# Kernel tuning notes

Hardware: AMD Instinct MI355X
Metric: run time of the kernel (lower is better)

## Reference

```python
import jax, jax.numpy as jnp
import numpy as np

D_MODEL = 1024
D_INNER = 2048  # expand * d_model
D_STATE = 16
D_CONV = 4
DT_RANK = 64    # ceil(d_model / 16)
B_SZ, L_SEQ = 2, 1024


def setup_inputs() -> dict:
    key = jax.random.key(0)
    ks = jax.random.split(key, 8)
    s = lambda fan_in: 1.0 / np.sqrt(fan_in)
    x = jax.random.normal(ks[0], (B_SZ, L_SEQ, D_MODEL), dtype=jnp.float32)
    in_proj_w = jax.random.normal(ks[1], (2 * D_INNER, D_MODEL), jnp.float32) * s(D_MODEL)
    conv_w = jax.random.normal(ks[2], (D_INNER, 1, D_CONV), jnp.float32) * s(D_CONV)
    conv_b = jax.random.normal(ks[3], (D_INNER,), jnp.float32) * 0.02
    x_proj_w = jax.random.normal(ks[4], (DT_RANK + 2 * D_STATE, D_INNER), jnp.float32) * s(D_INNER)
    dt_proj_w = jax.random.normal(ks[5], (D_INNER, DT_RANK), jnp.float32) * s(DT_RANK)
    dt_proj_b = jax.random.normal(ks[6], (D_INNER,), jnp.float32) * 0.02
    A_log = jnp.broadcast_to(jnp.log(jnp.arange(1, D_STATE + 1, dtype=jnp.float32)), (D_INNER, D_STATE))
    D_param = jnp.ones((D_INNER,), jnp.float32)
    out_proj_w = jax.random.normal(ks[7], (D_MODEL, D_INNER), jnp.float32) * s(D_INNER)
    return dict(x=x, in_proj_w=in_proj_w, conv_w=conv_w, conv_b=conv_b,
                x_proj_w=x_proj_w, dt_proj_w=dt_proj_w, dt_proj_b=dt_proj_b,
                A_log=A_log, D_param=D_param, out_proj_w=out_proj_w)


def _mamba_forward(x, in_proj_w, conv_w, conv_b, x_proj_w, dt_proj_w, dt_proj_b, A_log, D_param, out_proj_w):
    B, L, _ = x.shape
    # in_proj: (B,L,2*d_inner) -> split into conv branch and gate
    xz = jnp.einsum('bld,ed->ble', x, in_proj_w)
    x_br, z = jnp.split(xz, 2, axis=-1)
    # depthwise causal conv1d (left pad d_conv-1, truncate to L == torch pad+slice)
    xc = jnp.transpose(x_br, (0, 2, 1))  # (B, d_inner, L)
    xc = jax.lax.conv_general_dilated(
        xc, conv_w, window_strides=(1,), padding=[(D_CONV - 1, 0)],
        dimension_numbers=('NCH', 'OIH', 'NCH'), feature_group_count=D_INNER)
    xc = xc + conv_b[None, :, None]
    u = jax.nn.silu(jnp.transpose(xc, (0, 2, 1)))  # (B, L, d_inner) = SSM input
    # input-dependent params
    proj = jnp.einsum('bld,ed->ble', u, x_proj_w)
    delta_raw, B_in, C_in = jnp.split(proj, [DT_RANK, DT_RANK + D_STATE], axis=-1)
    delta = jax.nn.softplus(jnp.einsum('blr,dr->bld', delta_raw, dt_proj_w) + dt_proj_b)
    A = -jnp.exp(A_log)  # (d_inner, d_state)

    def step(h, inp):
        d_t, b_t, c_t, u_t = inp  # (B,d_inner),(B,d_state),(B,d_state),(B,d_inner)
        dA = jnp.exp(d_t[:, :, None] * A)                       # (B,d_inner,d_state)
        h = dA * h + (d_t * u_t)[:, :, None] * b_t[:, None, :]  # ZOH-ish update
        y_t = jnp.einsum('bds,bs->bd', h, c_t) + D_param * u_t
        return h, y_t

    h0 = jnp.zeros((B, D_INNER, D_STATE), dtype=x.dtype)
    inputs = (jnp.swapaxes(delta, 0, 1), jnp.swapaxes(B_in, 0, 1),
              jnp.swapaxes(C_in, 0, 1), jnp.swapaxes(u, 0, 1))
    _, ys = jax.lax.scan(step, h0, inputs)  # (L, B, d_inner)
    y = jnp.swapaxes(ys, 0, 1) * jax.nn.silu(z)
    return jnp.einsum('ble,de->bld', y, out_proj_w)


def reference(x, in_proj_w, conv_w, conv_b, x_proj_w, dt_proj_w, dt_proj_b, A_log, D_param, out_proj_w):
    return _mamba_forward(x, in_proj_w, conv_w, conv_b, x_proj_w, dt_proj_w, dt_proj_b, A_log, D_param, out_proj_w)
```

## Files before the change

kernel.cpp:

```cpp
#include <hip/hip_runtime.h>
#include <hip/hip_bf16.h>

#define D_MODEL 1024
#define D_INNER 2048
#define D_STATE 16
#define D_CONV  4
#define DT_RANK 64
#define B_SZ    2
#define L_SEQ   1024
#define BL      (B_SZ * L_SEQ)
#define NPROJ   (DT_RANK + 2 * D_STATE)
#define CS      32
#define NC      (L_SEQ / CS)

typedef __attribute__((ext_vector_type(8))) short bf16x8;
typedef __attribute__((ext_vector_type(4))) float floatx4;
typedef unsigned short ushort_t;

__device__ __forceinline__ void mfma_bf16(floatx4& acc, bf16x8 a, bf16x8 b) {
    asm volatile("v_mfma_f32_16x16x32_bf16 %0, %1, %2, %0"
                 : "+v"(acc) : "v"(a), "v"(b));
}

__device__ __forceinline__ void cvt_hilo(float f, ushort_t& hi, ushort_t& lo) {
    __hip_bfloat16 h = __float2bfloat16(f);
    hi = *(ushort_t*)&h;
    __hip_bfloat16 l = __float2bfloat16(f - __bfloat162float(h));
    lo = *(ushort_t*)&l;
}

__device__ __forceinline__ void cvt_store4(float4 v, ushort_t* hi, ushort_t* lo) {
    ushort4 h, l;
    cvt_hilo(v.x, h.x, l.x);
    cvt_hilo(v.y, h.y, l.y);
    cvt_hilo(v.z, h.z, l.z);
    cvt_hilo(v.w, h.w, l.w);
    *(ushort4*)hi = h;
    *(ushort4*)lo = l;
}

#define N4_WI 1048576
#define N4_WO 524288
#define N4_WD 32768
#define N4_X  524288

__global__ __launch_bounds__(256) void cvt_static(
    const float* __restrict__ wi, ushort_t* wihi, ushort_t* wilo,
    const float* __restrict__ wo, ushort_t* wohi, ushort_t* wolo,
    const float* __restrict__ wd, ushort_t* wdhi, ushort_t* wdlo,
    const float* __restrict__ x,  ushort_t* xhi,  ushort_t* xlo)
{
    int i = blockIdx.x * 256 + threadIdx.x;
    const float* src; ushort_t *dh, *dl;
    if (i < N4_WI)                         { src = wi; dh = wihi; dl = wilo; }
    else if ((i -= N4_WI) < N4_WO)         { src = wo; dh = wohi; dl = wolo; }
    else if ((i -= N4_WO) < N4_WD)         { src = wd; dh = wdhi; dl = wdlo; }
    else { i -= N4_WD;                       src = x;  dh = xhi;  dl = xlo;  }
    float4 v = ((const float4*)src)[i];
    cvt_store4(v, dh + i * 4, dl + i * 4);
}

template <int TM, int TN, int EPI, int CVTA, int KSPLIT>
__global__ __launch_bounds__(256, 2) void gemm_pre(
    const ushort_t* __restrict__ Ahi, const ushort_t* __restrict__ Alo, int lda,
    const float* __restrict__ Af, int ldaf,
    const ushort_t* __restrict__ Bhi, const ushort_t* __restrict__ Blo, int ldb,
    float* __restrict__ C, int ldc, int K,
    const float* __restrict__ bias)
{
    constexpr int LDT = 32;
    constexpr int IT = TM / 32, JT = TN / 32;
    __shared__ __align__(16) ushort_t As[2][TM * LDT];
    __shared__ __align__(16) ushort_t Bs[2][TN * LDT];

    const int tid = threadIdx.x;
    const int bm = blockIdx.y * TM;
    const int bn = blockIdx.x * TN;
    const int kstart = (KSPLIT > 1) ? blockIdx.z * (K / KSPLIT) : 0;
    const int kend   = (KSPLIT > 1) ? kstart + K / KSPLIT : K;

    const int wave = tid >> 6;
    const int lane = tid & 63;
    const int wm = (wave >> 1) * (TM / 2);
    const int wn = (wave & 1) * (TN / 2);
    const int ml = lane & 15;
    const int q  = lane >> 4;

    floatx4 acc[IT][JT];
#pragma unroll
    for (int i = 0; i < IT; ++i)
#pragma unroll
        for (int j = 0; j < JT; ++j) acc[i][j] = (floatx4)0.f;

    for (int k0 = kstart; k0 < kend; k0 += 32) {
        __syncthreads();
        if (CVTA) {
            const int r  = tid >> 1;
            const int kh = (tid & 1) * 16;
            const int sw = (r >> 1) & 3;
            const int c0 = (tid & 1) * 2;
            ushort_t hi[16], lo[16];
#pragma unroll
            for (int c = 0; c < 4; ++c) {
                float4 v = *(const float4*)(Af + (size_t)(bm + r) * ldaf + k0 + kh + c * 4);
                cvt_store4(v, hi + c * 4, lo + c * 4);
            }
            const int p0 = (c0 ^ sw) * 8;
            const int p1 = ((c0 + 1) ^ sw) * 8;
            *(uint4*)&As[0][r * LDT + p0] = *(uint4*)(hi + 0);
            *(uint4*)&As[0][r * LDT + p1] = *(uint4*)(hi + 8);
            *(uint4*)&As[1][r * LDT + p0] = *(uint4*)(lo + 0);
            *(uint4*)&As[1][r * LDT + p1] = *(uint4*)(lo + 8);
        } else {
#pragma unroll
            for (int ci = 0; ci < TM / 64; ++ci) {
                const int flat = tid + 256 * ci;
                const int r = flat >> 2, c = flat & 3;
                const int p = (c ^ ((r >> 1) & 3)) * 8;
                *(uint4*)&As[0][r * LDT + p] =
                    *(const uint4*)(Ahi + (size_t)(bm + r) * lda + k0 + c * 8);
                *(uint4*)&As[1][r * LDT + p] =
                    *(const uint4*)(Alo + (size_t)(bm + r) * lda + k0 + c * 8);
            }
        }
#pragma unroll
        for (int ci = 0; ci < TN / 64; ++ci) {
            const int flat = tid + 256 * ci;
            const int r = flat >> 2, c = flat & 3;
            const int p = (c ^ ((r >> 1) & 3)) * 8;
            *(uint4*)&Bs[0][r * LDT + p] =
                *(const uint4*)(Bhi + (size_t)(bn + r) * ldb + k0 + c * 8);
            *(uint4*)&Bs[1][r * LDT + p] =
                *(const uint4*)(Blo + (size_t)(bn + r) * ldb + k0 + c * 8);
        }
        __syncthreads();

        bf16x8 ah[IT], al[IT], bh[JT], bl[JT];
#pragma unroll
        for (int i = 0; i < IT; ++i) {
            const int r = wm + i * 16 + ml;
            const int p = (q ^ ((r >> 1) & 3)) * 8;
            ah[i] = *(const bf16x8*)&As[0][r * LDT + p];
            al[i] = *(const bf16x8*)&As[1][r * LDT + p];
        }
#pragma unroll
        for (int j = 0; j < JT; ++j) {
            const int r = wn + j * 16 + ml;
            const int p = (q ^ ((r >> 1) & 3)) * 8;
            bh[j] = *(const bf16x8*)&Bs[0][r * LDT + p];
            bl[j] = *(const bf16x8*)&Bs[1][r * LDT + p];
        }
#pragma unroll
        for (int i = 0; i < IT; ++i)
#pragma unroll
            for (int j = 0; j < JT; ++j) {
                mfma_bf16(acc[i][j], ah[i], bh[j]);
                mfma_bf16(acc[i][j], ah[i], bl[j]);
                mfma_bf16(acc[i][j], al[i], bh[j]);
            }
    }

    asm volatile("s_nop 7\n\ts_nop 7\n\ts_nop 7" ::: "memory");

#pragma unroll
    for (int i = 0; i < IT; ++i)
#pragma unroll
        for (int j = 0; j < JT; ++j)
#pragma unroll
            for (int r = 0; r < 4; ++r) {
                const int row = bm + wm + i * 16 + q * 4 + r;
                const int col = bn + wn + j * 16 + ml;
                float v = acc[i][j][r];
                if (KSPLIT > 1) {
                    atomicAdd(C + (size_t)row * ldc + col, v);
                } else {
                    if (EPI == 1) {
                        v += bias[col];
                        v = (v > 20.f) ? v : log1pf(__expf(v));
                    }
                    C[(size_t)row * ldc + col] = v;
                }
            }
}

#define PKC 128
#define PSC 64

__global__ __launch_bounds__(256) void gemm_proj_conv(
    const float* __restrict__ xz,
    const float* __restrict__ conv_w,
    const float* __restrict__ conv_b,
    const float* __restrict__ Wp,
    float* __restrict__ proj,
    float* __restrict__ u_out)
{
    __shared__ float us[PSC][65];
    __shared__ float wsh[PSC][100];

    const int tid = threadIdx.x;
    const int bm = blockIdx.y * 64;
    const int kbase0 = blockIdx.x * PKC;

    const int tx = tid & 15;
    const int ty = tid >> 4;

    float acc[4][6];
#pragma unroll
    for (int i = 0; i < 4; ++i)
#pragma unroll
        for (int j = 0; j < 6; ++j) acc[i][j] = 0.f;

    for (int sc = 0; sc < PKC / PSC; ++sc) {
        const int kb = kbase0 + sc * PSC;
        __syncthreads();
#pragma unroll
        for (int i = 0; i < 4; ++i) {
            const int flat = tid + 256 * i;
            const int r  = flat >> 4;
            const int kk = (flat & 15) * 4;
            const int k  = kb + kk;
            const int rr = bm + r;
            const int t  = rr & (L_SEQ - 1);
            const float* base = xz + (size_t)rr * 4096 + k;
            float4 x0 = *(const float4*)(base);
            float4 x1 = (t >= 1) ? *(const float4*)(base - 4096)  : make_float4(0,0,0,0);
            float4 x2 = (t >= 2) ? *(const float4*)(base - 8192)  : make_float4(0,0,0,0);
            float4 x3 = (t >= 3) ? *(const float4*)(base - 12288) : make_float4(0,0,0,0);
            float4 cb = *(const float4*)(conv_b + k);
            float4 w0 = ((const float4*)conv_w)[k + 0];
            float4 w1 = ((const float4*)conv_w)[k + 1];
            float4 w2 = ((const float4*)conv_w)[k + 2];
            float4 w3 = ((const float4*)conv_w)[k + 3];
            float4 uo;
            { float a = cb.x + w0.x*x3.x + w0.y*x2.x + w0.z*x1.x + w0.w*x0.x;
              uo.x = a / (1.f + __expf(-a)); }
            { float a = cb.y + w1.x*x3.y + w1.y*x2.y + w1.z*x1.y + w1.w*x0.y;
              uo.y = a / (1.f + __expf(-a)); }
            { float a = cb.z + w2.x*x3.z + w2.y*x2.z + w2.z*x1.z + w2.w*x0.z;
              uo.z = a / (1.f + __expf(-a)); }
            { float a = cb.w + w3.x*x3.w + w3.y*x2.w + w3.z*x1.w + w3.w*x0.w;
              uo.w = a / (1.f + __expf(-a)); }
            us[kk + 0][r] = uo.x;
            us[kk + 1][r] = uo.y;
            us[kk + 2][r] = uo.z;
            us[kk + 3][r] = uo.w;
            *(float4*)(u_out + (size_t)rr * D_INNER + k) = uo;
        }
#pragma unroll
        for (int i = 0; i < 6; ++i) {
            const int flat = tid + 256 * i;
            const int r = flat >> 4;
            const int k4 = flat & 15;
            float4 v = *(const float4*)(Wp + (size_t)r * D_INNER + kb + k4 * 4);
            wsh[k4*4+0][r] = v.x; wsh[k4*4+1][r] = v.y;
            wsh[k4*4+2][r] = v.z; wsh[k4*4+3][r] = v.w;
        }
        __syncthreads();

#pragma unroll 8
        for (int kk = 0; kk < PSC; ++kk) {
            float a[4], b[6];
#pragma unroll
            for (int i = 0; i < 4; ++i) a[i] = us[kk][ty * 4 + i];
#pragma unroll
            for (int j = 0; j < 6; ++j) b[j] = wsh[kk][tx + 16 * j];
#pragma unroll
            for (int i = 0; i < 4; ++i)
#pragma unroll
                for (int j = 0; j < 6; ++j) acc[i][j] += a[i] * b[j];
        }
    }

#pragma unroll
    for (int i = 0; i < 4; ++i)
#pragma unroll
        for (int j = 0; j < 6; ++j)
            atomicAdd(proj + (size_t)(bm + ty * 4 + i) * NPROJ + tx + 16 * j,
                      acc[i][j]);
}

__global__ __launch_bounds__(256) void scan_phase_a(
    const float* __restrict__ xz,
    const float* __restrict__ u,
    const float* __restrict__ proj,
    const float* __restrict__ A_log,
    float* __restrict__ hloc,
    float* __restrict__ sumd)
{
    const int d = blockIdx.x * 256 + threadIdx.x;
    const int c = blockIdx.y;
    const int b = blockIdx.z;

    float a[D_STATE];
#pragma unroll
    for (int s = 0; s < D_STATE; ++s) a[s] = -__expf(A_log[d * D_STATE + s]);

    float h[D_STATE];
#pragma unroll
    for (int s = 0; s < D_STATE; ++s) h[s] = 0.f;
    float sd = 0.f;

    for (int t = c * CS; t < (c + 1) * CS; ++t) {
        const size_t bt = (size_t)b * L_SEQ + t;
        const float dv = xz[bt * (2 * D_INNER) + d];
        const float uv = u[bt * D_INNER + d];
        const float du = dv * uv;
        sd += dv;
        const float* pr = proj + bt * NPROJ;
#pragma unroll
        for (int s = 0; s < D_STATE; ++s)
            h[s] = __expf(dv * a[s]) * h[s] + du * pr[DT_RANK + s];
    }

    const size_t base = ((size_t)(b * NC + c) * D_STATE) * D_INNER + d;
#pragma unroll
    for (int s = 0; s < D_STATE; ++s) hloc[base + (size_t)s * D_INNER] = h[s];
    sumd[(size_t)(b * NC + c) * D_INNER + d] = sd;
}

__global__ __launch_bounds__(256) void scan_phase_b(
    const float* __restrict__ hloc,
    const float* __restrict__ sumd,
    const float* __restrict__ A_log,
    float* __restrict__ carry)
{
    const int d = blockIdx.x * 256 + threadIdx.x;
    const int b = blockIdx.y;

    float a[D_STATE];
#pragma unroll
    for (int s = 0; s < D_STATE; ++s) a[s] = -__expf(A_log[d * D_STATE + s]);

    float hc[D_STATE];
#pragma unroll
    for (int s = 0; s < D_STATE; ++s) {
        hc[s] = 0.f;
        carry[((size_t)(b * NC + 0) * D_STATE + s) * D_INNER + d] = 0.f;
    }

    for (int c = 1; c < NC; ++c) {
        const float sd = sumd[(size_t)(b * NC + c - 1) * D_INNER + d];
        const size_t pbase = ((size_t)(b * NC + c - 1) * D_STATE) * D_INNER + d;
        const size_t cbase = ((size_t)(b * NC + c) * D_STATE) * D_INNER + d;
#pragma unroll
        for (int s = 0; s < D_STATE; ++s) {
            const float P = __expf(a[s] * sd);
            hc[s] = P * hc[s] + hloc[pbase + (size_t)s * D_INNER];
            carry[cbase + (size_t)s * D_INNER] = hc[s];
        }
    }
}

__global__ __launch_bounds__(256) void scan_phase_c(
    const float* __restrict__ xz,
    const float* __restrict__ u,
    const float* __restrict__ proj,
    const float* __restrict__ A_log,
    const float* __restrict__ D_param,
    const float* __restrict__ carry,
    ushort_t* __restrict__ Yhi,
    ushort_t* __restrict__ Ylo)
{
    const int d = blockIdx.x * 256 + threadIdx.x;
    const int c = blockIdx.y;
    const int b = blockIdx.z;

    float a[D_STATE];
#pragma unroll
    for (int s = 0; s < D_STATE; ++s) a[s] = -__expf(A_log[d * D_STATE + s]);
    const float Dp = D_param[d];

    float h[D_STATE];
    const size_t cbase = ((size_t)(b * NC + c) * D_STATE) * D_INNER + d;
#pragma unroll
    for (int s = 0; s < D_STATE; ++s) h[s] = carry[cbase + (size_t)s * D_INNER];

    for (int t = c * CS; t < (c + 1) * CS; ++t) {
        const size_t bt = (size_t)b * L_SEQ + t;
        const float dv = xz[bt * (2 * D_INNER) + d];
        const float uv = u[bt * D_INNER + d];
        const float du = dv * uv;
        const float* pr = proj + bt * NPROJ;

        float acc = 0.f;
#pragma unroll
        for (int s = 0; s < D_STATE; ++s) {
            h[s] = __expf(dv * a[s]) * h[s] + du * pr[DT_RANK + s];
            acc += h[s] * pr[DT_RANK + D_STATE + s];
        }
        const float yv = acc + Dp * uv;

        const float zv = xz[bt * (2 * D_INNER) + D_INNER + d];
        const float gate = zv / (1.f + __expf(-zv));
        ushort_t hh, ll;
        cvt_hilo(yv * gate, hh, ll);
        Yhi[bt * D_INNER + d] = hh;
        Ylo[bt * D_INNER + d] = ll;
    }
}

extern "C" void kernel_launch(void* const* d_in, const int* in_sizes, int n_in,
                              void* d_out, int out_size, void* d_ws, size_t ws_size,
                              hipStream_t stream)
{
    const float* x         = (const float*)d_in[0];
    const float* in_proj_w = (const float*)d_in[1];
    const float* conv_w    = (const float*)d_in[2];
    const float* conv_b    = (const float*)d_in[3];
    const float* x_proj_w  = (const float*)d_in[4];
    const float* dt_proj_w = (const float*)d_in[5];
    const float* dt_proj_b = (const float*)d_in[6];
    const float* A_log     = (const float*)d_in[7];
    const float* D_param   = (const float*)d_in[8];
    const float* out_proj_w= (const float*)d_in[9];
    float* out = (float*)d_out;

    float* xz    = (float*)d_ws;
    float* u     = xz    + (size_t)BL * 4096;
    float* proj  = u     + (size_t)BL * 2048;
    float* sumd  = proj  + (size_t)BL * NPROJ;
    float* carry = sumd  + (size_t)B_SZ * NC * D_INNER;
    ushort_t* Wihi = (ushort_t*)(carry + (size_t)B_SZ * NC * D_STATE * D_INNER);
    ushort_t* Wilo = Wihi + (size_t)4096 * 1024;
    ushort_t* Wohi = Wilo + (size_t)4096 * 1024;
    ushort_t* Wolo = Wohi + (size_t)1024 * 2048;
    ushort_t* Wdhi = Wolo + (size_t)1024 * 2048;
    ushort_t* Wdlo = Wdhi + (size_t)2048 * 64;
    ushort_t* Xhi  = (ushort_t*)carry;
    ushort_t* Xlo  = Xhi + (size_t)BL * D_MODEL;
    float*    hloc = (float*)Wihi;
    ushort_t* Yhi  = Wihi;
    ushort_t* Ylo  = Wilo;

    dim3 blk(256);

    cvt_static<<<(N4_WI + N4_WO + N4_WD + N4_X) / 256, blk, 0, stream>>>(
        in_proj_w, Wihi, Wilo, out_proj_w, Wohi, Wolo,
        dt_proj_w, Wdhi, Wdlo, x, Xhi, Xlo);

    gemm_pre<128, 128, 0, 0, 1><<<dim3(4096 / 128, BL / 128), blk, 0, stream>>>(
        Xhi, Xlo, D_MODEL, nullptr, 0, Wihi, Wilo, D_MODEL,
        xz, 2 * D_INNER, D_MODEL, nullptr);

    hipMemsetAsync(proj, 0, (size_t)BL * NPROJ * sizeof(float), stream);
    gemm_proj_conv<<<dim3(D_INNER / PKC, BL / 64), blk, 0, stream>>>(
        xz, conv_w, conv_b, x_proj_w, proj, u);

    gemm_pre<128, 128, 1, 1, 1><<<dim3(D_INNER / 128, BL / 128), blk, 0, stream>>>(
        nullptr, nullptr, 0, proj, NPROJ, Wdhi, Wdlo, DT_RANK,
        xz, 2 * D_INNER, DT_RANK, dt_proj_b);

    scan_phase_a<<<dim3(D_INNER / 256, NC, B_SZ), blk, 0, stream>>>(
        xz, u, proj, A_log, hloc, sumd);
    scan_phase_b<<<dim3(D_INNER / 256, B_SZ), blk, 0, stream>>>(
        hloc, sumd, A_log, carry);
    scan_phase_c<<<dim3(D_INNER / 256, NC, B_SZ), blk, 0, stream>>>(
        xz, u, proj, A_log, D_param, carry, Yhi, Ylo);

    hipMemsetAsync(out, 0, (size_t)BL * D_MODEL * sizeof(float), stream);
    gemm_pre<128, 64, 0, 0, 2><<<dim3(D_MODEL / 64, BL / 128, 2), blk, 0, stream>>>(
        Yhi, Ylo, D_INNER, nullptr, 0, Wohi, Wolo, D_INNER,
        out, D_MODEL, D_INNER, nullptr);
}
```

Baseline: 337.4 us.

## Replace dt_proj MFMA GEMM with FP32 delta kernel and fuse zero fills

Swaps the split-bf16 MFMA GEMM for dt_proj (K=64), which converted proj to hi/lo inside the tile loader, for a plain FP32 kernel. Each thread keeps one dt_proj_w row in registers, loops over 16 staged proj rows, and applies bias and softplus. It also drops the dt_proj_w conversion from cvt_static and merges the two memset calls into one zero-fill kernel at the start. The goal is to cut launch and conversion overhead on a small-K GEMM. The cost is the 64-float register array per thread, and the FP32 FMAs run on vector ALUs instead of MFMA.

```diff
diff --git a/kernel.cpp b/kernel.cpp
--- a/kernel.cpp
+++ b/kernel.cpp
@@ -39,34 +39,41 @@
     *(ushort4*)lo = l;
 }
 
+#define Z4_PROJ (BL * NPROJ / 4)
+#define Z4_OUT  (BL * D_MODEL / 4)
+
+__global__ __launch_bounds__(256) void zero_buf(float* __restrict__ proj,
+                                                float* __restrict__ out)
+{
+    int i = blockIdx.x * 256 + threadIdx.x;
+    float4 z = make_float4(0.f, 0.f, 0.f, 0.f);
+    if (i < Z4_PROJ) ((float4*)proj)[i] = z;
+    else             ((float4*)out)[i - Z4_PROJ] = z;
+}
+
 #define N4_WI 1048576
 #define N4_WO 524288
-#define N4_WD 32768
 #define N4_X  524288
 
 __global__ __launch_bounds__(256) void cvt_static(
     const float* __restrict__ wi, ushort_t* wihi, ushort_t* wilo,
     const float* __restrict__ wo, ushort_t* wohi, ushort_t* wolo,
-    const float* __restrict__ wd, ushort_t* wdhi, ushort_t* wdlo,
     const float* __restrict__ x,  ushort_t* xhi,  ushort_t* xlo)
 {
     int i = blockIdx.x * 256 + threadIdx.x;
     const float* src; ushort_t *dh, *dl;
-    if (i < N4_WI)                         { src = wi; dh = wihi; dl = wilo; }
-    else if ((i -= N4_WI) < N4_WO)         { src = wo; dh = wohi; dl = wolo; }
-    else if ((i -= N4_WO) < N4_WD)         { src = wd; dh = wdhi; dl = wdlo; }
-    else { i -= N4_WD;                       src = x;  dh = xhi;  dl = xlo;  }
+    if (i < N4_WI)                 { src = wi; dh = wihi; dl = wilo; }
+    else if ((i -= N4_WI) < N4_WO) { src = wo; dh = wohi; dl = wolo; }
+    else { i -= N4_WO;               src = x;  dh = xhi;  dl = xlo;  }
     float4 v = ((const float4*)src)[i];
     cvt_store4(v, dh + i * 4, dl + i * 4);
 }
 
-template <int TM, int TN, int EPI, int CVTA, int KSPLIT>
+template <int TM, int TN, int KSPLIT>
 __global__ __launch_bounds__(256, 2) void gemm_pre(
     const ushort_t* __restrict__ Ahi, const ushort_t* __restrict__ Alo, int lda,
-    const float* __restrict__ Af, int ldaf,
     const ushort_t* __restrict__ Bhi, const ushort_t* __restrict__ Blo, int ldb,
-    float* __restrict__ C, int ldc, int K,
-    const float* __restrict__ bias)
+    float* __restrict__ C, int ldc, int K)
 {
     constexpr int LDT = 32;
     constexpr int IT = TM / 32, JT = TN / 32;
@@ -94,34 +101,15 @@
 
     for (int k0 = kstart; k0 < kend; k0 += 32) {
         __syncthreads();
-        if (CVTA) {
-            const int r  = tid >> 1;
-            const int kh = (tid & 1) * 16;
-            const int sw = (r >> 1) & 3;
-            const int c0 = (tid & 1) * 2;
-            ushort_t hi[16], lo[16];
-#pragma unroll
-            for (int c = 0; c < 4; ++c) {
-                float4 v = *(const float4*)(Af + (size_t)(bm + r) * ldaf + k0 + kh + c * 4);
-                cvt_store4(v, hi + c * 4, lo + c * 4);
-            }
-            const int p0 = (c0 ^ sw) * 8;
-            const int p1 = ((c0 + 1) ^ sw) * 8;
-            *(uint4*)&As[0][r * LDT + p0] = *(uint4*)(hi + 0);
-            *(uint4*)&As[0][r * LDT + p1] = *(uint4*)(hi + 8);
-            *(uint4*)&As[1][r * LDT + p0] = *(uint4*)(lo + 0);
-            *(uint4*)&As[1][r * LDT + p1] = *(uint4*)(lo + 8);
-        } else {
-#pragma unroll
-            for (int ci = 0; ci < TM / 64; ++ci) {
-                const int flat = tid + 256 * ci;
-                const int r = flat >> 2, c = flat & 3;
-                const int p = (c ^ ((r >> 1) & 3)) * 8;
-                *(uint4*)&As[0][r * LDT + p] =
-                    *(const uint4*)(Ahi + (size_t)(bm + r) * lda + k0 + c * 8);
-                *(uint4*)&As[1][r * LDT + p] =
-                    *(const uint4*)(Alo + (size_t)(bm + r) * lda + k0 + c * 8);
-            }
+#pragma unroll
+        for (int ci = 0; ci < TM / 64; ++ci) {
+            const int flat = tid + 256 * ci;
+            const int r = flat >> 2, c = flat & 3;
+            const int p = (c ^ ((r >> 1) & 3)) * 8;
+            *(uint4*)&As[0][r * LDT + p] =
+                *(const uint4*)(Ahi + (size_t)(bm + r) * lda + k0 + c * 8);
+            *(uint4*)&As[1][r * LDT + p] =
+                *(const uint4*)(Alo + (size_t)(bm + r) * lda + k0 + c * 8);
         }
 #pragma unroll
         for (int ci = 0; ci < TN / 64; ++ci) {
@@ -170,17 +158,49 @@
             for (int r = 0; r < 4; ++r) {
                 const int row = bm + wm + i * 16 + q * 4 + r;
                 const int col = bn + wn + j * 16 + ml;
-                float v = acc[i][j][r];
-                if (KSPLIT > 1) {
-                    atomicAdd(C + (size_t)row * ldc + col, v);
-                } else {
-                    if (EPI == 1) {
-                        v += bias[col];
-                        v = (v > 20.f) ? v : log1pf(__expf(v));
-                    }
-                    C[(size_t)row * ldc + col] = v;
-                }
+                if (KSPLIT > 1)
+                    atomicAdd(C + (size_t)row * ldc + col, acc[i][j][r]);
+                else
+                    C[(size_t)row * ldc + col] = acc[i][j][r];
             }
+}
+
+__global__ __launch_bounds__(256) void delta_kernel(
+    const float* __restrict__ proj,
+    const float* __restrict__ Wd,
+    const float* __restrict__ bias,
+    float* __restrict__ xz)
+{
+    __shared__ float ps[16][65];
+    const int d  = blockIdx.x * 256 + threadIdx.x;
+    const int r0 = blockIdx.y * 16;
+
+    {
+        const int rr = threadIdx.x >> 4;
+        const int cc = (threadIdx.x & 15) * 4;
+        float4 v = *(const float4*)(proj + (size_t)(r0 + rr) * NPROJ + cc);
+        ps[rr][cc + 0] = v.x; ps[rr][cc + 1] = v.y;
+        ps[rr][cc + 2] = v.z; ps[rr][cc + 3] = v.w;
+    }
+    __syncthreads();
+
+    float w[64];
+#pragma unroll
+    for (int c4 = 0; c4 < 16; ++c4) {
+        float4 v = *(const float4*)(Wd + (size_t)d * 64 + c4 * 4);
+        w[c4 * 4 + 0] = v.x; w[c4 * 4 + 1] = v.y;
+        w[c4 * 4 + 2] = v.z; w[c4 * 4 + 3] = v.w;
+    }
+    const float bv = bias[d];
+
+#pragma unroll
+    for (int rr = 0; rr < 16; ++rr) {
+        float acc = bv;
+#pragma unroll
+        for (int k = 0; k < 64; ++k) acc += ps[rr][k] * w[k];
+        acc = (acc > 20.f) ? acc : log1pf(__expf(acc));
+        xz[(size_t)(r0 + rr) * 4096 + d] = acc;
+    }
 }
 
 #define PKC 128
@@ -424,8 +444,6 @@
     ushort_t* Wilo = Wihi + (size_t)4096 * 1024;
     ushort_t* Wohi = Wilo + (size_t)4096 * 1024;
     ushort_t* Wolo = Wohi + (size_t)1024 * 2048;
-    ushort_t* Wdhi = Wolo + (size_t)1024 * 2048;
-    ushort_t* Wdlo = Wdhi + (size_t)2048 * 64;
     ushort_t* Xhi  = (ushort_t*)carry;
     ushort_t* Xlo  = Xhi + (size_t)BL * D_MODEL;
     float*    hloc = (float*)Wihi;
@@ -434,21 +452,19 @@
 
     dim3 blk(256);
 
-    cvt_static<<<(N4_WI + N4_WO + N4_WD + N4_X) / 256, blk, 0, stream>>>(
-        in_proj_w, Wihi, Wilo, out_proj_w, Wohi, Wolo,
-        dt_proj_w, Wdhi, Wdlo, x, Xhi, Xlo);
-
-    gemm_pre<128, 128, 0, 0, 1><<<dim3(4096 / 128, BL / 128), blk, 0, stream>>>(
-        Xhi, Xlo, D_MODEL, nullptr, 0, Wihi, Wilo, D_MODEL,
-        xz, 2 * D_INNER, D_MODEL, nullptr);
-
-    hipMemsetAsync(proj, 0, (size_t)BL * NPROJ * sizeof(float), stream);
+    zero_buf<<<(Z4_PROJ + Z4_OUT + 255) / 256, blk, 0, stream>>>(proj, out);
+
+    cvt_static<<<(N4_WI + N4_WO + N4_X) / 256, blk, 0, stream>>>(
+        in_proj_w, Wihi, Wilo, out_proj_w, Wohi, Wolo, x, Xhi, Xlo);
+
+    gemm_pre<128, 128, 1><<<dim3(4096 / 128, BL / 128), blk, 0, stream>>>(
+        Xhi, Xlo, D_MODEL, Wihi, Wilo, D_MODEL, xz, 2 * D_INNER, D_MODEL);
+
     gemm_proj_conv<<<dim3(D_INNER / PKC, BL / 64), blk, 0, stream>>>(
         xz, conv_w, conv_b, x_proj_w, proj, u);
 
-    gemm_pre<128, 128, 1, 1, 1><<<dim3(D_INNER / 128, BL / 128), blk, 0, stream>>>(
-        nullptr, nullptr, 0, proj, NPROJ, Wdhi, Wdlo, DT_RANK,
-        xz, 2 * D_INNER, DT_RANK, dt_proj_b);
+    delta_kernel<<<dim3(D_INNER / 256, BL / 16), blk, 0, stream>>>(
+        proj, dt_proj_w, dt_proj_b, xz);
 
     scan_phase_a<<<dim3(D_INNER / 256, NC, B_SZ), blk, 0, stream>>>(
         xz, u, proj, A_log, hloc, sumd);
@@ -457,8 +473,6 @@
     scan_phase_c<<<dim3(D_INNER / 256, NC, B_SZ), blk, 0, stream>>>(
         xz, u, proj, A_log, D_param, carry, Yhi, Ylo);
 
-    hipMemsetAsync(out, 0, (size_t)BL * D_MODEL * sizeof(float), stream);
-    gemm_pre<128, 64, 0, 0, 2><<<dim3(D_MODEL / 64, BL / 128, 2), blk, 0, stream>>>(
-        Yhi, Ylo, D_INNER, nullptr, 0, Wohi, Wolo, D_INNER,
-        out, D_MODEL, D_INNER, nullptr);
-}
+    gemm_pre<128, 64, 2><<<dim3(D_MODEL / 64, BL / 128, 2), blk, 0, stream>>>(
+        Yhi, Ylo, D_INNER, Wohi, Wolo, D_INNER, out, D_MODEL, D_INNER);
+}
```

Result: faster. 327.5 us (-2.9%).
